# Optimization experiments

Hardware: AMD Instinct MI355X
Metric: run time of the kernel (lower is better)

Reference implementation:

```python
import jax, jax.numpy as jnp
import numpy as np

D_MODEL = 1024
H = 16
D_K = D_MODEL // H
BAND = 100  # attention allowed where |i-j| < BAND


def setup_inputs() -> dict:
    key = jax.random.key(0)
    ks = jax.random.split(key, 9)
    B, S = 2, 2048
    s = 1.0 / np.sqrt(D_MODEL)
    return {
        "x": jax.random.normal(ks[0], (B, S, D_MODEL), jnp.float32),
        "Wq": jax.random.normal(ks[1], (D_MODEL, D_MODEL), jnp.float32) * s,
        "bq": jnp.zeros((D_MODEL,), jnp.float32),
        "Wk": jax.random.normal(ks[2], (D_MODEL, D_MODEL), jnp.float32) * s,
        "bk": jnp.zeros((D_MODEL,), jnp.float32),
        "Wv": jax.random.normal(ks[3], (D_MODEL, D_MODEL), jnp.float32) * s,
        "bv": jnp.zeros((D_MODEL,), jnp.float32),
        "Wo": jax.random.normal(ks[4], (D_MODEL, D_MODEL), jnp.float32) * s,
        "bo": jnp.zeros((D_MODEL,), jnp.float32),
    }


def _split_heads(t, B, S):
    # [B, S, D] -> [B, H, S, D_K]
    return t.reshape(B, S, H, D_K).transpose(0, 2, 1, 3)


def reference(x, Wq, bq, Wk, bk, Wv, bv, Wo, bo):
    B, S, _ = x.shape
    q = _split_heads(x @ Wq.T + bq, B, S)
    k = _split_heads(x @ Wk.T + bk, B, S)
    v = _split_heads(x @ Wv.T + bv, B, S)

    scores = jnp.einsum("bhqd,bhkd->bhqk", q, k) / jnp.sqrt(jnp.float32(D_K))
    i = jnp.arange(S)
    band = jnp.abs(i[:, None] - i[None, :]) < BAND  # [S, S] True inside band
    scores = jnp.where(band[None, None, :, :], scores, jnp.float32(-1e9))
    p_attn = jax.nn.softmax(scores, axis=-1)

    out = jnp.einsum("bhqk,bhkd->bhqd", p_attn, v)
    out = out.transpose(0, 2, 1, 3).reshape(B, S, D_MODEL)
    return out @ Wo.T + bo
```

## Files before the change

kernel.cpp:

```cpp
#include <hip/hip_runtime.h>
#include <hip/hip_bf16.h>


typedef __attribute__((ext_vector_type(8))) short short8;
typedef __attribute__((ext_vector_type(4))) float f32x4;

#define S_LEN 2048
#define NH 16
#define DK 64
#define BANDW 100

#define X_ELEMS   (2 * S_LEN * 1024)
#define W_ELEMS   (1024 * 1024)
#define QKV_ELEMS (2 * NH * S_LEN * DK)
#define AO_ELEMS  (2 * S_LEN * 1024)

__device__ __attribute__((aligned(256))) short g_X[X_ELEMS];
__device__ __attribute__((aligned(256))) short g_W[4 * W_ELEMS];
__device__ __attribute__((aligned(256))) short g_b[4 * 1024];
__device__ __attribute__((aligned(256))) short g_Q[QKV_ELEMS];
__device__ __attribute__((aligned(256))) short g_K[QKV_ELEMS];
__device__ __attribute__((aligned(256))) short g_V[QKV_ELEMS];
__device__ __attribute__((aligned(256))) short g_AO[AO_ELEMS];

__device__ __forceinline__ float bf2f(short u) {
    unsigned x = ((unsigned)(unsigned short)u) << 16;
    return __builtin_bit_cast(float, x);
}
__device__ __forceinline__ short f2bf(float f) {
    unsigned x = __builtin_bit_cast(unsigned, f);
    unsigned r = (x + 0x7fffu + ((x >> 16) & 1u)) >> 16;
    return (short)r;
}

#define GLOAD_LDS(gp, lp) \
    __builtin_amdgcn_global_load_lds( \
        (const __attribute__((address_space(1))) void*)(gp), \
        (__attribute__((address_space(3))) void*)(lp), 16, 0, 0)

#define XC   (X_ELEMS / 8)
#define WC   (W_ELEMS / 8)
#define BC   (1024 / 8)
#define TOTC (XC + 4 * WC + 4 * BC)

__global__ __launch_bounds__(256) void convert_all(
    const void* __restrict__ x,
    const void* __restrict__ w0, const void* __restrict__ b0,
    const void* __restrict__ w1, const void* __restrict__ b1,
    const void* __restrict__ w2, const void* __restrict__ b2,
    const void* __restrict__ w3, const void* __restrict__ b3)
{
    int local = 0;
    {
        const unsigned* xw = (const unsigned*)x;
        #pragma unroll
        for (int i = 0; i < 4; i++) {
            unsigned wv = xw[(threadIdx.x & 63) * 4 + i];
            unsigned e = (wv >> 7) & 0xFF;
            if (e >= 100 && e <= 140) local++;
        }
    }
    const int is_bf16 = (__popcll(__ballot(local == 4)) > 32);

    long i = (long)blockIdx.x * 256 + threadIdx.x;
    if (i >= TOTC) return;

    const void* src; short* dst; long off;
    if (i < XC)                { src = x;  dst = g_X;              off = i; }
    else if ((i -= XC) < WC)   { src = w0; dst = g_W + 0L*W_ELEMS; off = i; }
    else if ((i -= WC) < WC)   { src = w1; dst = g_W + 1L*W_ELEMS; off = i; }
    else if ((i -= WC) < WC)   { src = w2; dst = g_W + 2L*W_ELEMS; off = i; }
    else if ((i -= WC) < WC)   { src = w3; dst = g_W + 3L*W_ELEMS; off = i; }
    else if ((i -= WC) < BC)   { src = b0; dst = g_b + 0*1024;     off = i; }
    else if ((i -= BC) < BC)   { src = b1; dst = g_b + 1*1024;     off = i; }
    else if ((i -= BC) < BC)   { src = b2; dst = g_b + 2*1024;     off = i; }
    else                       { src = b3; dst = g_b + 3*1024;     off = i - BC; }

    if (is_bf16) {
        ((short8*)dst)[off] = ((const short8*)src)[off];
    } else {
        const float* s = (const float*)src + off * 8;
        short8 o;
        #pragma unroll
        for (int e = 0; e < 8; e++) o[e] = f2bf(s[e]);
        ((short8*)dst)[off] = o;
    }
}

__global__ __launch_bounds__(256) void qkv_gemm()
{
    __shared__ __attribute__((aligned(16))) short As[128 * 64];
    __shared__ __attribute__((aligned(16))) short Bs[128 * 64];

    const int z = blockIdx.z;
    const short* __restrict__ X = g_X;
    const short* __restrict__ W = g_W + (long)z * W_ELEMS;
    const short* __restrict__ bias = g_b + z * 1024;
    short* __restrict__ Out = (z == 0) ? g_Q : ((z == 1) ? g_K : g_V);

    const int t = threadIdx.x;
    const int lane = t & 63;
    const int wid  = t >> 6;
    const int wm = wid & 1, wn = wid >> 1;
    const int l15 = lane & 15;
    const int g   = lane >> 4;
    const int mb = blockIdx.x * 128;
    const int nb = blockIdx.y * 128;

    long gA[4], gB[4];
    #pragma unroll
    for (int i = 0; i < 4; i++) {
        const int R = i * 32 + (t >> 3);
        const int l = (t & 7) ^ (R & 7);
        gA[i] = (long)(mb + R) * 1024 + l * 8;
        gB[i] = (long)(nb + R) * 1024 + l * 8;
    }
    short* lA = As + t * 8;
    short* lB = Bs + t * 8;

    f32x4 acc[4][4] = {};

    for (int k0 = 0; k0 < 1024; k0 += 64) {
        __syncthreads();
        #pragma unroll
        for (int i = 0; i < 4; i++) GLOAD_LDS(X + gA[i] + k0, lA + i * 2048);
        #pragma unroll
        for (int i = 0; i < 4; i++) GLOAD_LDS(W + gB[i] + k0, lB + i * 2048);
        __syncthreads();

        #pragma unroll
        for (int kh = 0; kh < 2; kh++) {
            short8 a[4], b[4];
            #pragma unroll
            for (int mt = 0; mt < 4; mt++) {
                const int r = wm * 64 + mt * 16 + l15;
                const int phys = (g + kh * 4) ^ (r & 7);
                a[mt] = *(const short8*)(As + r * 64 + phys * 8);
            }
            #pragma unroll
            for (int nt = 0; nt < 4; nt++) {
                const int r = wn * 64 + nt * 16 + l15;
                const int phys = (g + kh * 4) ^ (r & 7);
                b[nt] = *(const short8*)(Bs + r * 64 + phys * 8);
            }
            #pragma unroll
            for (int mt = 0; mt < 4; mt++)
                #pragma unroll
                for (int nt = 0; nt < 4; nt++)
                    acc[mt][nt] = __builtin_amdgcn_mfma_f32_16x16x32_bf16(a[mt], b[nt], acc[mt][nt], 0, 0, 0);
        }
    }

    const int rg = g * 4;
    #pragma unroll
    for (int nt = 0; nt < 4; nt++) {
        const int col = nb + wn * 64 + nt * 16 + l15;
        const float bv_ = bf2f(bias[col]);
        const int h = col >> 6, d = col & 63;
        #pragma unroll
        for (int mt = 0; mt < 4; mt++) {
            #pragma unroll
            for (int r = 0; r < 4; r++) {
                const int row = mb + wm * 64 + mt * 16 + rg + r;
                const int bI = row >> 11, s = row & 2047;
                Out[(((long)(bI * NH + h) * S_LEN) + s) * DK + d] = f2bf(acc[mt][nt][r] + bv_);
            }
        }
    }
}

__global__ __launch_bounds__(256) void o_gemm(float* __restrict__ Out)
{
    __shared__ __attribute__((aligned(16))) short As[128 * 32];
    __shared__ __attribute__((aligned(16))) short Bs[64 * 32];

    const short* __restrict__ A = g_AO;
    const short* __restrict__ W = g_W + 3L * W_ELEMS;

    const int t = threadIdx.x;
    const int lane = t & 63;
    const int wid  = t >> 6;
    const int wm = wid & 1, wn = wid >> 1;
    const int l15 = lane & 15;
    const int q8  = (lane >> 4) * 8;
    const int mb = blockIdx.x * 128;
    const int nb = blockIdx.y * 64;

    const long ga0 = (long)(mb + (t >> 2)) * 1024 + (t & 3) * 8;
    const long ga1 = (long)(mb + 64 + (t >> 2)) * 1024 + (t & 3) * 8;
    const long gb0 = (long)(nb + (t >> 2)) * 1024 + (t & 3) * 8;
    short* lA0 = As + t * 8;
    short* lA1 = As + 2048 + t * 8;
    short* lB0 = Bs + t * 8;

    f32x4 acc[4][2] = {};

    for (int k0 = 0; k0 < 1024; k0 += 32) {
        __syncthreads();
        GLOAD_LDS(A + ga0 + k0, lA0);
        GLOAD_LDS(A + ga1 + k0, lA1);
        GLOAD_LDS(W + gb0 + k0, lB0);
        __syncthreads();

        short8 a[4], b[2];
        #pragma unroll
        for (int mt = 0; mt < 4; mt++) a[mt] = *(const short8*)(As + (wm * 64 + mt * 16 + l15) * 32 + q8);
        #pragma unroll
        for (int nt = 0; nt < 2; nt++) b[nt] = *(const short8*)(Bs + (wn * 32 + nt * 16 + l15) * 32 + q8);
        #pragma unroll
        for (int mt = 0; mt < 4; mt++)
            #pragma unroll
            for (int nt = 0; nt < 2; nt++)
                acc[mt][nt] = __builtin_amdgcn_mfma_f32_16x16x32_bf16(a[mt], b[nt], acc[mt][nt], 0, 0, 0);
    }

    const int rg = (lane >> 4) * 4;
    #pragma unroll
    for (int nt = 0; nt < 2; nt++) {
        const int col = nb + wn * 32 + nt * 16 + l15;
        const float bv_ = bf2f(g_b[3 * 1024 + col]);
        #pragma unroll
        for (int mt = 0; mt < 4; mt++) {
            #pragma unroll
            for (int r = 0; r < 4; r++) {
                const int row = mb + wm * 64 + mt * 16 + rg + r;
                Out[(long)row * 1024 + col] = acc[mt][nt][r] + bv_;
            }
        }
    }
}

#define VT_PAD 328

__global__ __launch_bounds__(256) void attn_kernel()
{
    __shared__ __attribute__((aligned(16))) short Vt[64][VT_PAD];
    __shared__ __attribute__((aligned(16))) short Pl[4][16][72];

    const int bid  = blockIdx.x;
    const int head = bid & 31;
    const int qt   = bid >> 5;
    const int h = head & 15, b = head >> 4;
    const int qbase = qt * 64;

    const int lane = threadIdx.x & 63;
    const int w    = threadIdx.x >> 6;
    const int l15  = lane & 15;
    const int qg   = lane >> 4;
    const int q8   = qg * 8;

    const long hoff = (long)(b * NH + h) * S_LEN * DK;
    const short* __restrict__ Qh = g_Q + hoff;
    const short* __restrict__ Kh = g_K + hoff;
    const short* __restrict__ Vh = g_V + hoff;

    const int lo  = qbase - (BANDW - 1);
    const int kc0 = (lo < 0 ? 0 : lo) >> 6;
    int hi = qbase + 64 + (BANDW - 1);
    if (hi > S_LEN) hi = S_LEN;
    const int kc1 = (hi + 63) >> 6;
    const int kb0 = kc0 * 64;
    const int nkc = kc1 - kc0;
    const int n_keys = nkc * 64;

    const short* qp = Qh + (long)(qbase + w * 16 + l15) * DK + q8;
    const short8 aq0 = *(const short8*)(qp);
    const short8 aq1 = *(const short8*)(qp + 32);

    const int npairs = n_keys >> 1;
    for (int u = threadIdx.x; u < npairs; u += 256) {
        const short* vp0 = Vh + (long)(kb0 + 2 * u) * DK;
        #pragma unroll
        for (int tq = 0; tq < 8; tq++) {
            const short8 v0 = *(const short8*)(vp0 + tq * 8);
            const short8 v1 = *(const short8*)(vp0 + DK + tq * 8);
            #pragma unroll
            for (int e = 0; e < 8; e++) {
                const int pk = (int)(unsigned short)v0[e] | ((int)(unsigned short)v1[e] << 16);
                *(int*)&Vt[tq * 8 + e][2 * u] = pk;
            }
        }
    }
    __syncthreads();

    f32x4 sc[5][4];
    float mx[4] = {-1e30f, -1e30f, -1e30f, -1e30f};
    #pragma unroll
    for (int c = 0; c < 5; c++) {
        const bool live = (c < nkc);
        const int kb = kb0 + (live ? c : 0) * 64;
        #pragma unroll
        for (int nt = 0; nt < 4; nt++) {
            const short* kp = Kh + (long)(kb + nt * 16 + l15) * DK + q8;
            const short8 bk0 = *(const short8*)(kp);
            const short8 bk1 = *(const short8*)(kp + 32);
            f32x4 z = {};
            z = __builtin_amdgcn_mfma_f32_16x16x32_bf16(aq0, bk0, z, 0, 0, 0);
            z = __builtin_amdgcn_mfma_f32_16x16x32_bf16(aq1, bk1, z, 0, 0, 0);
            const int kg = kb + nt * 16 + l15;
            #pragma unroll
            for (int r = 0; r < 4; r++) {
                const int qI = qbase + w * 16 + qg * 4 + r;
                int dlt = qI - kg; if (dlt < 0) dlt = -dlt;
                const float v = (live && dlt < BANDW) ? z[r] * 0.125f : -1e30f;
                sc[c][nt][r] = v;
                mx[r] = fmaxf(mx[r], v);
            }
        }
    }
    #pragma unroll
    for (int mk = 1; mk < 16; mk <<= 1)
        #pragma unroll
        for (int r = 0; r < 4; r++) mx[r] = fmaxf(mx[r], __shfl_xor(mx[r], mk, 64));

    float lsum[4] = {0.f, 0.f, 0.f, 0.f};
    #pragma unroll
    for (int c = 0; c < 5; c++)
        #pragma unroll
        for (int nt = 0; nt < 4; nt++)
            #pragma unroll
            for (int r = 0; r < 4; r++) {
                const float p = (sc[c][nt][r] > -0.5e30f)
                    ? __builtin_exp2f((sc[c][nt][r] - mx[r]) * 1.44269504f) : 0.f;
                sc[c][nt][r] = p;
                lsum[r] += p;
            }
    #pragma unroll
    for (int mk = 1; mk < 16; mk <<= 1)
        #pragma unroll
        for (int r = 0; r < 4; r++) lsum[r] += __shfl_xor(lsum[r], mk, 64);

    f32x4 o[4] = {};
    #pragma unroll
    for (int c = 0; c < 5; c++) {
        if (c >= nkc) break;
        const int kloc = c * 64;
        #pragma unroll
        for (int nt = 0; nt < 4; nt++)
            #pragma unroll
            for (int r = 0; r < 4; r++)
                Pl[w][qg * 4 + r][nt * 16 + l15] = f2bf(sc[c][nt][r]);
        asm volatile("s_waitcnt lgkmcnt(0)" ::: "memory");
        const short8 ap0 = *(const short8*)(&Pl[w][l15][q8]);
        const short8 ap1 = *(const short8*)(&Pl[w][l15][32 + q8]);

        #pragma unroll
        for (int nt2 = 0; nt2 < 4; nt2++) {
            const short* vrow = &Vt[nt2 * 16 + l15][kloc];
            const short8 bv0 = *(const short8*)(vrow + q8);
            const short8 bv1 = *(const short8*)(vrow + 32 + q8);
            o[nt2] = __builtin_amdgcn_mfma_f32_16x16x32_bf16(ap0, bv0, o[nt2], 0, 0, 0);
            o[nt2] = __builtin_amdgcn_mfma_f32_16x16x32_bf16(ap1, bv1, o[nt2], 0, 0, 0);
        }
    }

    #pragma unroll
    for (int nt2 = 0; nt2 < 4; nt2++)
        #pragma unroll
        for (int r = 0; r < 4; r++) {
            const int qI = qbase + w * 16 + qg * 4 + r;
            const int d = nt2 * 16 + l15;
            g_AO[((long)b * S_LEN + qI) * 1024 + h * DK + d] = f2bf(o[nt2][r] / lsum[r]);
        }
}

extern "C" void kernel_launch(void* const* d_in, const int* in_sizes, int n_in,
                              void* d_out, int out_size, void* d_ws, size_t ws_size,
                              hipStream_t stream) {
    float* out = (float*)d_out;

    convert_all<<<(TOTC + 255) / 256, 256, 0, stream>>>(
        d_in[0], d_in[1], d_in[2], d_in[3], d_in[4], d_in[5], d_in[6], d_in[7], d_in[8]);
    qkv_gemm<<<dim3(32, 8, 3), 256, 0, stream>>>();
    attn_kernel<<<dim3(2 * NH * (S_LEN / 64)), 256, 0, stream>>>();
    o_gemm<<<dim3(32, 16), 256, 0, stream>>>(out);
}
```

Before: 184.7 us.

## Process 128 queries per attention block with online softmax over key chunks

```diff
diff --git a/kernel.cpp b/kernel.cpp
--- a/kernel.cpp
+++ b/kernel.cpp
@@ -230,7 +230,7 @@
     }
 }
 
-#define VT_PAD 328
+#define VT_PAD 392
 
 __global__ __launch_bounds__(256) void attn_kernel()
 {
@@ -241,7 +241,7 @@
     const int head = bid & 31;
     const int qt   = bid >> 5;
     const int h = head & 15, b = head >> 4;
-    const int qbase = qt * 64;
+    const int qbase = qt * 128;
 
     const int lane = threadIdx.x & 63;
     const int w    = threadIdx.x >> 6;
@@ -256,16 +256,19 @@
 
     const int lo  = qbase - (BANDW - 1);
     const int kc0 = (lo < 0 ? 0 : lo) >> 6;
-    int hi = qbase + 64 + (BANDW - 1);
+    int hi = qbase + 128 + (BANDW - 1);
     if (hi > S_LEN) hi = S_LEN;
     const int kc1 = (hi + 63) >> 6;
     const int kb0 = kc0 * 64;
-    const int nkc = kc1 - kc0;
-    const int n_keys = nkc * 64;
-
-    const short* qp = Qh + (long)(qbase + w * 16 + l15) * DK + q8;
-    const short8 aq0 = *(const short8*)(qp);
-    const short8 aq1 = *(const short8*)(qp + 32);
+    const int n_keys = (kc1 - kc0) * 64;
+
+    short8 aq0[2], aq1[2];
+    #pragma unroll
+    for (int g2 = 0; g2 < 2; g2++) {
+        const short* qp = Qh + (long)(qbase + g2 * 64 + w * 16 + l15) * DK + q8;
+        aq0[g2] = *(const short8*)(qp);
+        aq1[g2] = *(const short8*)(qp + 32);
+    }
 
     const int npairs = n_keys >> 1;
     for (int u = threadIdx.x; u < npairs; u += 256) {
@@ -283,85 +286,116 @@
     }
     __syncthreads();
 
-    f32x4 sc[5][4];
-    float mx[4] = {-1e30f, -1e30f, -1e30f, -1e30f};
-    #pragma unroll
-    for (int c = 0; c < 5; c++) {
-        const bool live = (c < nkc);
-        const int kb = kb0 + (live ? c : 0) * 64;
+    f32x4 o[2][4] = {};
+    float m_r[2][4], l_r[2][4];
+    #pragma unroll
+    for (int g2 = 0; g2 < 2; g2++)
+        #pragma unroll
+        for (int r = 0; r < 4; r++) { m_r[g2][r] = -1e30f; l_r[g2][r] = 0.f; }
+
+    for (int kc = kc0; kc < kc1; kc++) {
+        const int kb = kc * 64;
+        const int kloc = kb - kb0;
+
+        short8 bk0[4], bk1[4];
         #pragma unroll
         for (int nt = 0; nt < 4; nt++) {
             const short* kp = Kh + (long)(kb + nt * 16 + l15) * DK + q8;
-            const short8 bk0 = *(const short8*)(kp);
-            const short8 bk1 = *(const short8*)(kp + 32);
-            f32x4 z = {};
-            z = __builtin_amdgcn_mfma_f32_16x16x32_bf16(aq0, bk0, z, 0, 0, 0);
-            z = __builtin_amdgcn_mfma_f32_16x16x32_bf16(aq1, bk1, z, 0, 0, 0);
-            const int kg = kb + nt * 16 + l15;
+            bk0[nt] = *(const short8*)(kp);
+            bk1[nt] = *(const short8*)(kp + 32);
+        }
+
+        #pragma unroll
+        for (int g2 = 0; g2 < 2; g2++) {
+            const int gqb = qbase + g2 * 64;
+            if (kb + 163 <= gqb || kb >= gqb + 163) continue;
+
+            f32x4 sc[4];
+            #pragma unroll
+            for (int nt = 0; nt < 4; nt++) {
+                f32x4 z = {};
+                z = __builtin_amdgcn_mfma_f32_16x16x32_bf16(aq0[g2], bk0[nt], z, 0, 0, 0);
+                z = __builtin_amdgcn_mfma_f32_16x16x32_bf16(aq1[g2], bk1[nt], z, 0, 0, 0);
+                sc[nt] = z;
+            }
+
+            float pv[4][4];
+            float mx[4] = {-1e30f, -1e30f, -1e30f, -1e30f};
+            #pragma unroll
+            for (int nt = 0; nt < 4; nt++) {
+                const int kg = kb + nt * 16 + l15;
+                #pragma unroll
+                for (int r = 0; r < 4; r++) {
+                    const int qI = gqb + w * 16 + qg * 4 + r;
+                    int dlt = qI - kg; if (dlt < 0) dlt = -dlt;
+                    const float v = (dlt < BANDW) ? sc[nt][r] * 0.125f : -1e30f;
+                    pv[nt][r] = v;
+                    mx[r] = fmaxf(mx[r], v);
+                }
+            }
+            #pragma unroll
+            for (int mk = 1; mk < 16; mk <<= 1)
+                #pragma unroll
+                for (int r = 0; r < 4; r++) mx[r] = fmaxf(mx[r], __shfl_xor(mx[r], mk, 64));
+
+            float alpha[4], lnew[4];
             #pragma unroll
             for (int r = 0; r < 4; r++) {
-                const int qI = qbase + w * 16 + qg * 4 + r;
-                int dlt = qI - kg; if (dlt < 0) dlt = -dlt;
-                const float v = (live && dlt < BANDW) ? z[r] * 0.125f : -1e30f;
-                sc[c][nt][r] = v;
-                mx[r] = fmaxf(mx[r], v);
-            }
-        }
-    }
-    #pragma unroll
-    for (int mk = 1; mk < 16; mk <<= 1)
-        #pragma unroll
-        for (int r = 0; r < 4; r++) mx[r] = fmaxf(mx[r], __shfl_xor(mx[r], mk, 64));
-
-    float lsum[4] = {0.f, 0.f, 0.f, 0.f};
-    #pragma unroll
-    for (int c = 0; c < 5; c++)
-        #pragma unroll
-        for (int nt = 0; nt < 4; nt++)
+                const float mn = fmaxf(m_r[g2][r], mx[r]);
+                alpha[r] = __builtin_exp2f((m_r[g2][r] - mn) * 1.44269504f);
+                m_r[g2][r] = mn;
+                lnew[r] = 0.f;
+            }
+            #pragma unroll
+            for (int nt = 0; nt < 4; nt++)
+                #pragma unroll
+                for (int r = 0; r < 4; r++) {
+                    const float p = (pv[nt][r] > -0.5e30f)
+                        ? __builtin_exp2f((pv[nt][r] - m_r[g2][r]) * 1.44269504f) : 0.f;
+                    pv[nt][r] = p;
+                    lnew[r] += p;
+                }
+            #pragma unroll
+            for (int mk = 1; mk < 16; mk <<= 1)
+                #pragma unroll
+                for (int r = 0; r < 4; r++) lnew[r] += __shfl_xor(lnew[r], mk, 64);
+            #pragma unroll
+            for (int r = 0; r < 4; r++) l_r[g2][r] = l_r[g2][r] * alpha[r] + lnew[r];
+            #pragma unroll
+            for (int nt2 = 0; nt2 < 4; nt2++)
+                #pragma unroll
+                for (int r = 0; r < 4; r++) o[g2][nt2][r] *= alpha[r];
+
+            #pragma unroll
+            for (int nt = 0; nt < 4; nt++)
+                #pragma unroll
+                for (int r = 0; r < 4; r++)
+                    Pl[w][qg * 4 + r][nt * 16 + l15] = f2bf(pv[nt][r]);
+            asm volatile("s_waitcnt lgkmcnt(0)" ::: "memory");
+            const short8 ap0 = *(const short8*)(&Pl[w][l15][q8]);
+            const short8 ap1 = *(const short8*)(&Pl[w][l15][32 + q8]);
+
+            #pragma unroll
+            for (int nt2 = 0; nt2 < 4; nt2++) {
+                const short* vrow = &Vt[nt2 * 16 + l15][kloc];
+                const short8 bv0 = *(const short8*)(vrow + q8);
+                const short8 bv1 = *(const short8*)(vrow + 32 + q8);
+                o[g2][nt2] = __builtin_amdgcn_mfma_f32_16x16x32_bf16(ap0, bv0, o[g2][nt2], 0, 0, 0);
+                o[g2][nt2] = __builtin_amdgcn_mfma_f32_16x16x32_bf16(ap1, bv1, o[g2][nt2], 0, 0, 0);
+            }
+        }
+    }
+
+    #pragma unroll
+    for (int g2 = 0; g2 < 2; g2++)
+        #pragma unroll
+        for (int nt2 = 0; nt2 < 4; nt2++)
             #pragma unroll
             for (int r = 0; r < 4; r++) {
-                const float p = (sc[c][nt][r] > -0.5e30f)
-                    ? __builtin_exp2f((sc[c][nt][r] - mx[r]) * 1.44269504f) : 0.f;
-                sc[c][nt][r] = p;
-                lsum[r] += p;
-            }
-    #pragma unroll
-    for (int mk = 1; mk < 16; mk <<= 1)
-        #pragma unroll
-        for (int r = 0; r < 4; r++) lsum[r] += __shfl_xor(lsum[r], mk, 64);
-
-    f32x4 o[4] = {};
-    #pragma unroll
-    for (int c = 0; c < 5; c++) {
-        if (c >= nkc) break;
-        const int kloc = c * 64;
-        #pragma unroll
-        for (int nt = 0; nt < 4; nt++)
-            #pragma unroll
-            for (int r = 0; r < 4; r++)
-                Pl[w][qg * 4 + r][nt * 16 + l15] = f2bf(sc[c][nt][r]);
-        asm volatile("s_waitcnt lgkmcnt(0)" ::: "memory");
-        const short8 ap0 = *(const short8*)(&Pl[w][l15][q8]);
-        const short8 ap1 = *(const short8*)(&Pl[w][l15][32 + q8]);
-
-        #pragma unroll
-        for (int nt2 = 0; nt2 < 4; nt2++) {
-            const short* vrow = &Vt[nt2 * 16 + l15][kloc];
-            const short8 bv0 = *(const short8*)(vrow + q8);
-            const short8 bv1 = *(const short8*)(vrow + 32 + q8);
-            o[nt2] = __builtin_amdgcn_mfma_f32_16x16x32_bf16(ap0, bv0, o[nt2], 0, 0, 0);
-            o[nt2] = __builtin_amdgcn_mfma_f32_16x16x32_bf16(ap1, bv1, o[nt2], 0, 0, 0);
-        }
-    }
-
-    #pragma unroll
-    for (int nt2 = 0; nt2 < 4; nt2++)
-        #pragma unroll
-        for (int r = 0; r < 4; r++) {
-            const int qI = qbase + w * 16 + qg * 4 + r;
-            const int d = nt2 * 16 + l15;
-            g_AO[((long)b * S_LEN + qI) * 1024 + h * DK + d] = f2bf(o[nt2][r] / lsum[r]);
-        }
+                const int qI = qbase + g2 * 64 + w * 16 + qg * 4 + r;
+                const int d = nt2 * 16 + l15;
+                g_AO[((long)b * S_LEN + qI) * 1024 + h * DK + d] = f2bf(o[g2][nt2][r] / l_r[g2][r]);
+            }
 }
 
 extern "C" void kernel_launch(void* const* d_in, const int* in_sizes, int n_in,
@@ -372,6 +406,6 @@
     convert_all<<<(TOTC + 255) / 256, 256, 0, stream>>>(
         d_in[0], d_in[1], d_in[2], d_in[3], d_in[4], d_in[5], d_in[6], d_in[7], d_in[8]);
     qkv_gemm<<<dim3(32, 8, 3), 256, 0, stream>>>();
-    attn_kernel<<<dim3(2 * NH * (S_LEN / 64)), 256, 0, stream>>>();
+    attn_kernel<<<dim3(2 * NH * (S_LEN / 128)), 256, 0, stream>>>();
     o_gemm<<<dim3(32, 16), 256, 0, stream>>>(out);
 }
```

Result: no change. 183.8 us (-0.5%).
